# Optimization experiments

Measured on AMD Instinct MI355X. Metric: run time of the kernel, lower is better.

## Reference

```python
import jax, jax.numpy as jnp
import numpy as np

B, N, C, H = 2, 2048, 1024, 16
D = C // H          # head dim = 64
HID = 4 * C         # MLP hidden = 4096
LN_EPS = 1e-5
ROPE_BASE = 10000.0


def layernorm(x, g, b):
    mu = jnp.mean(x, axis=-1, keepdims=True)
    var = jnp.var(x, axis=-1, keepdims=True)
    return (x - mu) * jax.lax.rsqrt(var + LN_EPS) * g + b


def rotate_half(x):
    # interleaved pairs: (x0, x1) -> (-x1, x0), lucidrains rotary_embedding_torch style
    x = x.reshape(*x.shape[:-1], -1, 2)
    x1, x2 = x[..., 0], x[..., 1]
    return jnp.stack([-x2, x1], axis=-1).reshape(*x.shape[:-2], -1)


def rope_cos_sin(n, d, dtype):
    inv_freq = 1.0 / (ROPE_BASE ** (jnp.arange(0, d, 2, dtype=jnp.float32) / d))
    ang = jnp.arange(n, dtype=jnp.float32)[:, None] * inv_freq          # [N, D/2]
    ang = jnp.repeat(ang, 2, axis=-1)                                    # [N, D] interleaved
    return jnp.cos(ang).astype(dtype), jnp.sin(ang).astype(dtype)


def setup_inputs() -> dict:
    key = jax.random.key(0)
    ks = jax.random.split(key, 16)
    s = 0.02
    return {
        "x": jax.random.normal(ks[0], (B, N, C), jnp.float32),
        "ln1_g": jnp.ones((C,), jnp.float32),
        "ln1_b": jnp.zeros((C,), jnp.float32),
        "qkv_w": jax.random.normal(ks[1], (C, 3 * C), jnp.float32) * s,   # stored [in, out]
        "qkv_b": jnp.zeros((3 * C,), jnp.float32),
        "proj_w": jax.random.normal(ks[2], (C, C), jnp.float32) * s,
        "proj_b": jnp.zeros((C,), jnp.float32),
        "ln2_g": jnp.ones((C,), jnp.float32),
        "ln2_b": jnp.zeros((C,), jnp.float32),
        "fc1_w": jax.random.normal(ks[3], (C, HID), jnp.float32) * s,
        "fc1_b": jnp.zeros((HID,), jnp.float32),
        "ffn_ln_g": jnp.ones((HID,), jnp.float32),
        "ffn_ln_b": jnp.zeros((HID,), jnp.float32),
        "fc2_w": jax.random.normal(ks[4], (HID, C), jnp.float32) * s,
        "fc2_b": jnp.zeros((C,), jnp.float32),
    }


def reference(x, ln1_g, ln1_b, qkv_w, qkv_b, proj_w, proj_b,
              ln2_g, ln2_b, fc1_w, fc1_b, ffn_ln_g, ffn_ln_b, fc2_w, fc2_b):
    b, n, c = x.shape
    h, d = H, c // H
    scale = d ** -0.5

    # --- attention branch (pre-norm) ---
    hx = layernorm(x, ln1_g, ln1_b)
    qkv = hx @ qkv_w + qkv_b                                   # [B,N,3C]
    qkv = qkv.reshape(b, n, 3, h, d).transpose(2, 0, 3, 1, 4)  # [3,B,H,N,D]
    q, k, v = qkv[0], qkv[1], qkv[2]

    cos, sin = rope_cos_sin(n, d, x.dtype)                     # [N,D]
    q = q * cos + rotate_half(q) * sin
    k = k * cos + rotate_half(k) * sin

    attn = jax.nn.softmax(jnp.einsum('bhqd,bhkd->bhqk', q, k) * scale, axis=-1)
    o = jnp.einsum('bhqk,bhkd->bhqd', attn, v)                 # [B,H,N,D]
    o = o.transpose(0, 2, 1, 3).reshape(b, n, c)               # B N (H D)
    x = x + o @ proj_w + proj_b

    # --- MLP branch (pre-norm; GELU then LayerNorm on hidden, per FeedForwardBlock) ---
    m = layernorm(x, ln2_g, ln2_b)
    m = jax.nn.gelu(m @ fc1_w + fc1_b, approximate=False)
    m = layernorm(m, ffn_ln_g, ffn_ln_b)
    m = m @ fc2_w + fc2_b
    return x + m
```

## Files before the change

### kernel.cpp

```cpp
#include <hip/hip_runtime.h>
#include <hip/hip_bf16.h>
#include <cmath>

typedef __bf16 bf16_t;
typedef __bf16 bf16x8 __attribute__((ext_vector_type(8)));
typedef float f32x4 __attribute__((ext_vector_type(4)));
typedef float f32x16 __attribute__((ext_vector_type(16)));
typedef unsigned short u16;
typedef unsigned int u32;
typedef unsigned int u32x2 __attribute__((ext_vector_type(2)));

#if defined(__has_builtin)
#if __has_builtin(__builtin_amdgcn_exp2f)
#define ATTN_EXP(x) __builtin_amdgcn_exp2f(x)
#define ATTN_LOG2E 1.4426950408889634f
#define HAVE_EXP2 1
#endif
#if __has_builtin(__builtin_amdgcn_permlane32_swap)
#define HAVE_PL32 1
#endif
#if __has_builtin(__builtin_amdgcn_rcpf)
#define FAST_RCP(x) __builtin_amdgcn_rcpf(x)
#endif
#endif
#ifndef ATTN_EXP
#define ATTN_EXP(x) __expf(x)
#define ATTN_LOG2E 1.0f
#endif
#ifndef FAST_RCP
#define FAST_RCP(x) (1.0f / (x))
#endif

__device__ __forceinline__ float fast_gelu(float v) {
#ifdef HAVE_EXP2
  float u = v * __builtin_fmaf(0.044715f, v * v, 1.0f);
  float z = __builtin_amdgcn_exp2f(-2.3022163968f * u);
  return v * FAST_RCP(1.0f + z);
#else
  return 0.5f * v * (1.0f + erff(v * 0.70710678118654752f));
#endif
}

__device__ __forceinline__ void load16(const bf16_t* g, bf16_t* l) {
  __builtin_amdgcn_global_load_lds((const __attribute__((address_space(1))) u32*)g,
                                   (__attribute__((address_space(3))) u32*)l, 16, 0, 0);
}

__device__ __forceinline__ u32 pk2(float a, float b) {
  bf16_t x = (bf16_t)a, y = (bf16_t)b;
  u16 ux = __builtin_bit_cast(u16, x), uy = __builtin_bit_cast(u16, y);
  return (u32)ux | ((u32)uy << 16);
}

union V4U { u32 w[4]; bf16x8 v; };

__device__ __forceinline__ void pl32(u32 a, u32 b, u32& out_lo, u32& out_hi) {
#ifdef HAVE_PL32
  u32x2 r = __builtin_amdgcn_permlane32_swap(a, b, false, false);
  out_lo = r[0];
  out_hi = r[1];
#else
  u32 ax = (u32)__shfl_xor((int)a, 32), bx = (u32)__shfl_xor((int)b, 32);
  out_lo = (threadIdx.x & 32) ? bx : a;
  out_hi = (threadIdx.x & 32) ? b : ax;
#endif
}

__device__ __forceinline__ float pl32_sum(float x) {
  u32 lo, hi;
  pl32(__builtin_bit_cast(u32, x), __builtin_bit_cast(u32, x), lo, hi);
  return __builtin_bit_cast(float, lo) + __builtin_bit_cast(float, hi);
}

__device__ __forceinline__ void tr64(const float* __restrict__ src, bf16_t* __restrict__ dst,
                                     int Kd, int Nd, int ntile, int ktile, int tid) {
  __shared__ float tile[64][68];
  int n0 = ntile * 64, k0 = ktile * 64;
  int r = tid >> 2, c4 = (tid & 3) * 4;
  const float* sp = src + (size_t)(k0 + r) * Nd + n0;
#pragma unroll
  for (int c = 0; c < 4; ++c)
    *(float4*)&tile[r][c * 16 + c4] = *(const float4*)(sp + c * 16 + c4);
  __syncthreads();
  int n = tid >> 2;
  bf16_t* dp = dst + (size_t)(n0 + n) * Kd + k0;
#pragma unroll
  for (int c = 0; c < 4; ++c) {
    int kk = c * 16 + c4;
    uint2 pk;
    pk.x = pk2(tile[kk + 0][n], tile[kk + 1][n]);
    pk.y = pk2(tile[kk + 2][n], tile[kk + 3][n]);
    *(uint2*)(dp + kk) = pk;
  }
}

__global__ __launch_bounds__(256) void prep_kernel(
    const float* __restrict__ qkv_w, const float* __restrict__ proj_w,
    const float* __restrict__ fc1_w, const float* __restrict__ fc2_w,
    bf16_t* __restrict__ qkvT, bf16_t* __restrict__ projT,
    bf16_t* __restrict__ fc1T, bf16_t* __restrict__ fc2T,
    float* __restrict__ ropeC, float* __restrict__ ropeS) {
  int b = blockIdx.x, tid = threadIdx.x;
  if (b < 768) {
    tr64(qkv_w, qkvT, 1024, 3072, b % 48, b / 48, tid);
  } else if (b < 1024) {
    int r = b - 768; tr64(proj_w, projT, 1024, 1024, r % 16, r / 16, tid);
  } else if (b < 2048) {
    int r = b - 1024; tr64(fc1_w, fc1T, 1024, 4096, r % 64, r / 64, tid);
  } else if (b < 3072) {
    int r = b - 2048; tr64(fc2_w, fc2T, 4096, 1024, r % 16, r / 16, tid);
  } else {
    int idx = (b - 3072) * 256 + tid;
    int pos = idx >> 5, t = idx & 31;
    float e = (float)(2 * t) / 64.0f;
    float inv = powf(10000.0f, -e);
    float a = (float)pos * inv;
    ropeC[idx] = cosf(a);
    ropeS[idx] = sinf(a);
  }
}

template <typename TI, int W>
__global__ __launch_bounds__(256) void ln_kernel(const TI* __restrict__ in,
                                                 const float* __restrict__ g,
                                                 const float* __restrict__ b,
                                                 bf16_t* __restrict__ out) {
  constexpr int CH = (sizeof(TI) == 2) ? 8 : 4;
  constexpr int NS = W / (256 * CH);
  int row = blockIdx.x;
  const TI* p = in + (size_t)row * W;
  float vals[NS * CH];
  float s = 0.f, q = 0.f;
#pragma unroll
  for (int sw = 0; sw < NS; ++sw) {
    int base = sw * (256 * CH) + threadIdx.x * CH;
    if constexpr (sizeof(TI) == 2) {
      bf16x8 v = *(const bf16x8*)(p + base);
#pragma unroll
      for (int e = 0; e < 8; ++e) {
        float f = (float)v[e];
        vals[sw * CH + e] = f; s += f; q += f * f;
      }
    } else {
      float4 v = *(const float4*)(p + base);
      float f0 = v.x, f1 = v.y, f2 = v.z, f3 = v.w;
      vals[sw * CH + 0] = f0; vals[sw * CH + 1] = f1;
      vals[sw * CH + 2] = f2; vals[sw * CH + 3] = f3;
      s += (f0 + f1) + (f2 + f3);
      q += (f0 * f0 + f1 * f1) + (f2 * f2 + f3 * f3);
    }
  }
  for (int off = 32; off; off >>= 1) { s += __shfl_xor(s, off); q += __shfl_xor(q, off); }
  __shared__ float red[8];
  int wave = threadIdx.x >> 6, lane = threadIdx.x & 63;
  if (lane == 0) { red[wave] = s; red[4 + wave] = q; }
  __syncthreads();
  s = red[0] + red[1] + red[2] + red[3];
  q = red[4] + red[5] + red[6] + red[7];
  float mu = s * (1.0f / W);
  float var = q * (1.0f / W) - mu * mu;
  float rstd = rsqrtf(var + 1e-5f);
  bf16_t* op = out + (size_t)row * W;
#pragma unroll
  for (int sw = 0; sw < NS; ++sw) {
    int base = sw * (256 * CH) + threadIdx.x * CH;
    float o[CH];
#pragma unroll
    for (int e = 0; e < CH; ++e)
      o[e] = (vals[sw * CH + e] - mu) * rstd * g[base + e] + b[base + e];
    if constexpr (CH == 8) {
      V4U u;
      u.w[0] = pk2(o[0], o[1]); u.w[1] = pk2(o[2], o[3]);
      u.w[2] = pk2(o[4], o[5]); u.w[3] = pk2(o[6], o[7]);
      *(bf16x8*)(op + base) = u.v;
    } else {
      uint2 pk; pk.x = pk2(o[0], o[1]); pk.y = pk2(o[2], o[3]);
      *(uint2*)(op + base) = pk;
    }
  }
}

template <int NS>
__global__ __launch_bounds__(256) void reduceN_kernel(
    const float* __restrict__ part, const float* __restrict__ resid,
    const float* __restrict__ bias, float* __restrict__ out) {
  const int total4 = (4096 * 1024) / 4;
  const float4* r4 = (const float4*)resid;
  const float4* b4 = (const float4*)bias;
  float4* o4 = (float4*)out;
  for (int i = blockIdx.x * 256 + threadIdx.x; i < total4; i += gridDim.x * 256) {
    float4 a = ((const float4*)part)[i];
#pragma unroll
    for (int s = 1; s < NS; ++s) {
      float4 p = ((const float4*)(part + (size_t)s * 4096 * 1024))[i];
      a.x += p.x; a.y += p.y; a.z += p.z; a.w += p.w;
    }
    float4 r = r4[i], bb = b4[i & 255];
    float4 o;
    o.x = a.x + (r.x + bb.x);
    o.y = a.y + (r.y + bb.y);
    o.z = a.z + (r.z + bb.z);
    o.w = a.w + (r.w + bb.w);
    o4[i] = o;
  }
}

enum { EPI_QKV = 0, EPI_RESID = 1, EPI_GELU = 2, EPI_PART = 3 };

template <int EPI, int TM>
__global__ __launch_bounds__(256, 2) void gemm_bt(
    const bf16_t* __restrict__ A, const bf16_t* __restrict__ Bt, int M, int Nn, int K,
    int gy, int ksteps,
    const float* __restrict__ bias, const float* __restrict__ resid,
    float* __restrict__ outf, bf16_t* __restrict__ outb,
    bf16_t* __restrict__ qb, bf16_t* __restrict__ kb, bf16_t* __restrict__ vtb,
    const float* __restrict__ ropeC, const float* __restrict__ ropeS) {
  constexpr int MT = TM / 32;
  __shared__ bf16_t lsA[2][TM * 32];
  __shared__ bf16_t lsB[2][128 * 32];
  const int tid = threadIdx.x;
  const int lane = tid & 63;
  const int wave = tid >> 6;
  const int l16 = lane & 15, quad = lane >> 4;
  const int wm = (wave >> 1) * (TM / 2), wn = (wave & 1) * 64;
  const int bb = blockIdx.x;
  const int m0 = (bb % gy) * TM, n0 = (bb / gy) * 128;
  const int kbase = blockIdx.y * (ksteps << 5);

  f32x4 acc[MT][4];
  for (int i = 0; i < MT; ++i)
    for (int j = 0; j < 4; ++j) acc[i][j] = {0.f, 0.f, 0.f, 0.f};

  auto stage = [&](int kk, int buf) {
    bf16_t* la = &lsA[buf][0];
    bf16_t* lb = &lsB[buf][0];
#pragma unroll
    for (int i = 0; i < TM / 64; ++i) {
      int s = tid + i * 256;
      int row = s >> 2, ch = (s & 3) ^ (row & 3);
      load16(A + (size_t)(m0 + row) * K + kk + ch * 8, la + s * 8);
    }
#pragma unroll
    for (int i = 0; i < 2; ++i) {
      int s = tid + i * 256;
      int row = s >> 2, ch = (s & 3) ^ (row & 3);
      load16(Bt + (size_t)(n0 + row) * K + kk + ch * 8, lb + s * 8);
    }
  };

  stage(kbase, 0);
  for (int ki = 0; ki < ksteps; ++ki) {
    __syncthreads();
    if (ki + 1 < ksteps) stage(kbase + ((ki + 1) << 5), (ki + 1) & 1);
    const bf16_t* la = &lsA[ki & 1][0];
    const bf16_t* lb = &lsB[ki & 1][0];
    bf16x8 af[MT], bfr[4];
#pragma unroll
    for (int t = 0; t < MT; ++t) {
      int row = wm + t * 16 + l16;
      af[t] = *(const bf16x8*)(la + row * 32 + (quad ^ (row & 3)) * 8);
    }
#pragma unroll
    for (int t = 0; t < 4; ++t) {
      int row = wn + t * 16 + l16;
      bfr[t] = *(const bf16x8*)(lb + row * 32 + (quad ^ (row & 3)) * 8);
    }
#pragma unroll
    for (int mt = 0; mt < MT; ++mt)
#pragma unroll
      for (int nt = 0; nt < 4; ++nt)
        acc[mt][nt] = __builtin_amdgcn_mfma_f32_16x16x32_bf16(af[mt], bfr[nt], acc[mt][nt], 0, 0, 0);
  }

  for (int mt = 0; mt < MT; ++mt) {
    for (int nt = 0; nt < 4; ++nt) {
      int gn = n0 + wn + nt * 16 + l16;
      int gm0 = m0 + wm + mt * 16 + quad * 4;
      if constexpr (EPI == EPI_QKV) {
        int which = gn >> 10;
        int hd = gn & 1023, head = hd >> 6, d = hd & 63;
        if (which == 2) {
          u32 lo, hi;
          {
            float v0 = acc[mt][nt][0] + bias[gn];
            float v1 = acc[mt][nt][1] + bias[gn];
            float v2 = acc[mt][nt][2] + bias[gn];
            float v3 = acc[mt][nt][3] + bias[gn];
            lo = pk2(v0, v1);
            hi = pk2(v2, v3);
          }
          int b = gm0 >> 11, pos = gm0 & 2047;
          int bh = b * 16 + head;
          uint2 pk; pk.x = lo; pk.y = hi;
          *(uint2*)(vtb + ((size_t)bh * 64 + d) * 2048 + pos) = pk;
        } else {
          bf16_t* dst = (which == 0) ? qb : kb;
          int t = d >> 1;
          for (int r = 0; r < 4; ++r) {
            float v = acc[mt][nt][r] + bias[gn];
            float pn = __shfl_xor(v, 1);
            int gm = gm0 + r;
            int b = gm >> 11, pos = gm & 2047;
            float cc = ropeC[pos * 32 + t], ss = ropeS[pos * 32 + t];
            float o = (d & 1) ? (v * cc + pn * ss) : (v * cc - pn * ss);
            dst[(((size_t)(b * 16 + head)) * 2048 + pos) * 64 + d] = (bf16_t)o;
          }
        }
      } else if constexpr (EPI == EPI_GELU) {
        for (int r = 0; r < 4; ++r) {
          int gm = gm0 + r;
          float v = acc[mt][nt][r] + bias[gn];
          outb[(size_t)gm * Nn + gn] = (bf16_t)fast_gelu(v);
        }
      } else if constexpr (EPI == EPI_PART) {
        float* po = outf + (size_t)blockIdx.y * M * Nn;
        for (int r = 0; r < 4; ++r) {
          int gm = gm0 + r;
          po[(size_t)gm * Nn + gn] = acc[mt][nt][r];
        }
      } else {
        for (int r = 0; r < 4; ++r) {
          int gm = gm0 + r;
          size_t idx = (size_t)gm * Nn + gn;
          outf[idx] = acc[mt][nt][r] + bias[gn] + resid[idx];
        }
      }
    }
  }
}

__global__ __launch_bounds__(256, 2) void attn_kernel(
    const bf16_t* __restrict__ q, const bf16_t* __restrict__ k,
    const bf16_t* __restrict__ vt, bf16_t* __restrict__ o) {
  __shared__ bf16_t lsK[2][128 * 64];
  __shared__ bf16_t lsV[2][64 * 128];

  const int tid = threadIdx.x, lane = tid & 63, wave = tid >> 6;
  const int c31 = lane & 31, hi = lane >> 5, h7 = c31 & 7;
  const int bh = blockIdx.y, qt = blockIdx.x;
  const int b = bh >> 4, h = bh & 15;
  const bf16_t* qp = q + (size_t)bh * 2048 * 64;
  const bf16_t* kp = k + (size_t)bh * 2048 * 64;
  const bf16_t* vp = vt + (size_t)bh * 64 * 2048;
  const int qrow0 = qt * 128 + wave * 32;
  const int qrow = qrow0 + c31;

  const float QS = 0.125f * ATTN_LOG2E;
  bf16x8 qb[4];
#pragma unroll
  for (int ks = 0; ks < 4; ++ks) {
    bf16x8 t = *(const bf16x8*)(qp + (size_t)qrow * 64 + ks * 16 + hi * 8);
#pragma unroll
    for (int j = 0; j < 8; ++j) t[j] = (bf16_t)((float)t[j] * QS);
    qb[ks] = t;
  }

  f32x16 oacc[2];
  oacc[0] = 0.f; oacc[1] = 0.f;
  float lstate = 0.f;

  auto stage = [&](int kt, int buf) {
    const bf16_t* kg = kp + (size_t)kt * 128 * 64;
    bf16_t* lk = &lsK[buf][0];
    bf16_t* lv = &lsV[buf][0];
#pragma unroll
    for (int i = 0; i < 4; ++i) {
      int s = tid + i * 256;
      int kr = s >> 3, kc = (s & 7) ^ (kr & 7);
      load16(kg + (size_t)kr * 64 + kc * 8, lk + s * 8);
      int vr = s >> 4, vc = (s & 15) ^ (vr & 7);
      load16(vp + (size_t)vr * 2048 + kt * 128 + vc * 8, lv + s * 8);
    }
  };

  stage(0, 0);
  for (int kt = 0; kt < 16; ++kt) {
    __syncthreads();
    if (kt < 15) stage(kt + 1, (kt + 1) & 1);
    const bf16_t* lk = &lsK[kt & 1][0];
    const bf16_t* lv = &lsV[kt & 1][0];

    f32x16 sacc[4];
    sacc[0] = 0.f; sacc[1] = 0.f; sacc[2] = 0.f; sacc[3] = 0.f;
    __builtin_amdgcn_s_setprio(1);
#pragma unroll
    for (int ks = 0; ks < 4; ++ks) {
      int cs = ((ks * 2 + hi) ^ h7) * 8;
#pragma unroll
      for (int nt = 0; nt < 4; ++nt) {
        bf16x8 kf = *(const bf16x8*)(lk + (nt * 32 + c31) * 64 + cs);
        sacc[nt] = __builtin_amdgcn_mfma_f32_32x32x16_bf16(kf, qb[ks], sacc[nt], 0, 0, 0);
      }
    }
    __builtin_amdgcn_s_setprio(0);

    float rsn[4];
    u32 u[4][4][2];
#pragma unroll
    for (int nt = 0; nt < 4; ++nt) {
      float a0 = 0.f, a1 = 0.f;
#pragma unroll
      for (int t = 0; t < 4; ++t) {
        float p0 = ATTN_EXP(sacc[nt][4 * t + 0]);
        float p1 = ATTN_EXP(sacc[nt][4 * t + 1]);
        float p2 = ATTN_EXP(sacc[nt][4 * t + 2]);
        float p3 = ATTN_EXP(sacc[nt][4 * t + 3]);
        a0 += p0 + p1; a1 += p2 + p3;
        u[nt][t][0] = pk2(p0, p1);
        u[nt][t][1] = pk2(p2, p3);
      }
      rsn[nt] = a0 + a1;
    }
    float rs = (rsn[0] + rsn[1]) + (rsn[2] + rsn[3]);
    rs = pl32_sum(rs);
    lstate += rs;

    __builtin_amdgcn_s_setprio(1);
#pragma unroll
    for (int ks = 0; ks < 8; ++ks) {
      int n = ks >> 1, t0 = (ks & 1) * 2;
      V4U f;
      pl32(u[n][t0][0], u[n][t0 + 1][0], f.w[0], f.w[2]);
      pl32(u[n][t0][1], u[n][t0 + 1][1], f.w[1], f.w[3]);
      bf16x8 pf = f.v;
      int cs = ((ks * 2 + hi) ^ h7) * 8;
#pragma unroll
      for (int dt = 0; dt < 2; ++dt) {
        bf16x8 vf = *(const bf16x8*)(lv + (dt * 32 + c31) * 128 + cs);
        oacc[dt] = __builtin_amdgcn_mfma_f32_32x32x16_bf16(vf, pf, oacc[dt], 0, 0, 0);
      }
    }
    __builtin_amdgcn_s_setprio(0);
  }

  float inv = 1.0f / lstate;
  bf16_t* orow = o + ((size_t)(b * 2048 + qrow)) * 1024 + h * 64;
#pragma unroll
  for (int dt = 0; dt < 2; ++dt)
#pragma unroll
    for (int t = 0; t < 4; ++t) {
      int d0 = dt * 32 + 8 * t + 4 * hi;
      uint2 pk;
      pk.x = pk2(oacc[dt][4 * t + 0] * inv, oacc[dt][4 * t + 1] * inv);
      pk.y = pk2(oacc[dt][4 * t + 2] * inv, oacc[dt][4 * t + 3] * inv);
      *(uint2*)(orow + d0) = pk;
    }
}

extern "C" void kernel_launch(void* const* d_in, const int* in_sizes, int n_in,
                              void* d_out, int out_size, void* d_ws, size_t ws_size,
                              hipStream_t stream) {
  const float* x = (const float*)d_in[0];
  const float* ln1_g = (const float*)d_in[1];
  const float* ln1_b = (const float*)d_in[2];
  const float* qkv_w = (const float*)d_in[3];
  const float* qkv_b = (const float*)d_in[4];
  const float* proj_w = (const float*)d_in[5];
  const float* proj_b = (const float*)d_in[6];
  const float* ln2_g = (const float*)d_in[7];
  const float* ln2_b = (const float*)d_in[8];
  const float* fc1_w = (const float*)d_in[9];
  const float* fc1_b = (const float*)d_in[10];
  const float* ffg = (const float*)d_in[11];
  const float* ffb = (const float*)d_in[12];
  const float* fc2_w = (const float*)d_in[13];
  const float* fc2_b = (const float*)d_in[14];
  float* out = (float*)d_out;

  char* ws = (char*)d_ws;
  size_t off = 0;
  auto alloc = [&](size_t n) { char* p = ws + off; off += (n + 255) & ~(size_t)255; return p; };

  bf16_t* qkvT  = (bf16_t*)alloc(3072ull * 1024 * 2);
  bf16_t* projT = (bf16_t*)alloc(1024ull * 1024 * 2);
  bf16_t* fc1T  = (bf16_t*)alloc(4096ull * 1024 * 2);
  bf16_t* fc2T  = (bf16_t*)alloc(1024ull * 4096 * 2);
  float*  ropeC = (float*)alloc(2048ull * 32 * 4);
  float*  ropeS = (float*)alloc(2048ull * 32 * 4);
  bf16_t* hx    = (bf16_t*)alloc(4096ull * 1024 * 2);
  bf16_t* qbuf  = (bf16_t*)alloc(32ull * 2048 * 64 * 2);
  bf16_t* kbuf  = (bf16_t*)alloc(32ull * 2048 * 64 * 2);
  bf16_t* vtbuf = (bf16_t*)alloc(32ull * 64 * 2048 * 2);
  bf16_t* obuf  = (bf16_t*)alloc(4096ull * 1024 * 2);
  float*  x2    = (float*)alloc(4096ull * 1024 * 4);
  bf16_t* h1    = (bf16_t*)alloc(4096ull * 4096 * 2);
  bf16_t* hln   = (bf16_t*)qbuf;

  const size_t part4_bytes = 4ull * 4096 * 1024 * 4;
  float* part;
  int nsplit;
  if (off + part4_bytes <= ws_size) {
    part = (float*)alloc(part4_bytes);
    nsplit = 4;
  } else {
    part = (float*)h1;
    nsplit = 2;
  }

  prep_kernel<<<3328, 256, 0, stream>>>(qkv_w, proj_w, fc1_w, fc2_w,
                                        qkvT, projT, fc1T, fc2T, ropeC, ropeS);

  ln_kernel<float, 1024><<<4096, 256, 0, stream>>>(x, ln1_g, ln1_b, hx);
  gemm_bt<EPI_QKV, 128><<<768, 256, 0, stream>>>(hx, qkvT, 4096, 3072, 1024, 32, 32, qkv_b,
      nullptr, nullptr, nullptr, qbuf, kbuf, vtbuf, ropeC, ropeS);
  attn_kernel<<<dim3(16, 32), 256, 0, stream>>>(qbuf, kbuf, vtbuf, obuf);
  gemm_bt<EPI_RESID, 64><<<512, 256, 0, stream>>>(obuf, projT, 4096, 1024, 1024, 64, 32,
      proj_b, x, x2, nullptr, nullptr, nullptr, nullptr, nullptr, nullptr);
  ln_kernel<float, 1024><<<4096, 256, 0, stream>>>(x2, ln2_g, ln2_b, hx);
  gemm_bt<EPI_GELU, 128><<<1024, 256, 0, stream>>>(hx, fc1T, 4096, 4096, 1024, 32, 32, fc1_b,
      nullptr, nullptr, h1, nullptr, nullptr, nullptr, nullptr, nullptr);
  ln_kernel<bf16_t, 4096><<<4096, 256, 0, stream>>>(h1, ffg, ffb, hln);
  gemm_bt<EPI_PART, 128><<<dim3(256, nsplit), 256, 0, stream>>>(hln, fc2T, 4096, 1024, 4096,
      32, 128 / nsplit, nullptr, nullptr, part, nullptr, nullptr, nullptr, nullptr,
      nullptr, nullptr);
  if (nsplit == 4)
    reduceN_kernel<4><<<2048, 256, 0, stream>>>(part, x2, fc2_b, out);
  else
    reduceN_kernel<2><<<2048, 256, 0, stream>>>(part, x2, fc2_b, out);
}
```

Before: 372.7 us.

## Single-buffer V in LDS via register staging to raise attention occupancy

```diff
diff --git a/kernel.cpp b/kernel.cpp
--- a/kernel.cpp
+++ b/kernel.cpp
@@ -329,11 +329,11 @@
   }
 }
 
-__global__ __launch_bounds__(256, 2) void attn_kernel(
+__global__ __launch_bounds__(256, 3) void attn_kernel(
     const bf16_t* __restrict__ q, const bf16_t* __restrict__ k,
     const bf16_t* __restrict__ vt, bf16_t* __restrict__ o) {
   __shared__ bf16_t lsK[2][128 * 64];
-  __shared__ bf16_t lsV[2][64 * 128];
+  __shared__ bf16_t lsV[64 * 128];
 
   const int tid = threadIdx.x, lane = tid & 63, wave = tid >> 6;
   const int c31 = lane & 31, hi = lane >> 5, h7 = c31 & 7;
@@ -359,26 +359,45 @@
   oacc[0] = 0.f; oacc[1] = 0.f;
   float lstate = 0.f;
 
-  auto stage = [&](int kt, int buf) {
+  auto stage_k = [&](int kt, int buf) {
     const bf16_t* kg = kp + (size_t)kt * 128 * 64;
     bf16_t* lk = &lsK[buf][0];
-    bf16_t* lv = &lsV[buf][0];
 #pragma unroll
     for (int i = 0; i < 4; ++i) {
       int s = tid + i * 256;
       int kr = s >> 3, kc = (s & 7) ^ (kr & 7);
       load16(kg + (size_t)kr * 64 + kc * 8, lk + s * 8);
+    }
+  };
+  auto load_v = [&](int kt, bf16x8* vr4) {
+#pragma unroll
+    for (int i = 0; i < 4; ++i) {
+      int s = tid + i * 256;
       int vr = s >> 4, vc = (s & 15) ^ (vr & 7);
-      load16(vp + (size_t)vr * 2048 + kt * 128 + vc * 8, lv + s * 8);
+      vr4[i] = *(const bf16x8*)(vp + (size_t)vr * 2048 + kt * 128 + vc * 8);
     }
   };
-
-  stage(0, 0);
+  auto write_v = [&](const bf16x8* vr4) {
+#pragma unroll
+    for (int i = 0; i < 4; ++i) {
+      int s = tid + i * 256;
+      *(bf16x8*)(&lsV[s * 8]) = vr4[i];
+    }
+  };
+
+  bf16x8 vreg[4];
+  stage_k(0, 0);
+  load_v(0, vreg);
+  __syncthreads();
+  write_v(vreg);
+  __syncthreads();
+
   for (int kt = 0; kt < 16; ++kt) {
-    __syncthreads();
-    if (kt < 15) stage(kt + 1, (kt + 1) & 1);
+    if (kt < 15) {
+      stage_k(kt + 1, (kt + 1) & 1);
+      load_v(kt + 1, vreg);
+    }
     const bf16_t* lk = &lsK[kt & 1][0];
-    const bf16_t* lv = &lsV[kt & 1][0];
 
     f32x16 sacc[4];
     sacc[0] = 0.f; sacc[1] = 0.f; sacc[2] = 0.f; sacc[3] = 0.f;
@@ -426,11 +445,17 @@
       int cs = ((ks * 2 + hi) ^ h7) * 8;
 #pragma unroll
       for (int dt = 0; dt < 2; ++dt) {
-        bf16x8 vf = *(const bf16x8*)(lv + (dt * 32 + c31) * 128 + cs);
+        bf16x8 vf = *(const bf16x8*)(&lsV[(dt * 32 + c31) * 128 + cs]);
         oacc[dt] = __builtin_amdgcn_mfma_f32_32x32x16_bf16(vf, pf, oacc[dt], 0, 0, 0);
       }
     }
     __builtin_amdgcn_s_setprio(0);
+
+    if (kt < 15) {
+      __syncthreads();
+      write_v(vreg);
+      __syncthreads();
+    }
   }
 
   float inv = 1.0f / lstate;
@@ -485,17 +510,7 @@
   float*  x2    = (float*)alloc(4096ull * 1024 * 4);
   bf16_t* h1    = (bf16_t*)alloc(4096ull * 4096 * 2);
   bf16_t* hln   = (bf16_t*)qbuf;
-
-  const size_t part4_bytes = 4ull * 4096 * 1024 * 4;
-  float* part;
-  int nsplit;
-  if (off + part4_bytes <= ws_size) {
-    part = (float*)alloc(part4_bytes);
-    nsplit = 4;
-  } else {
-    part = (float*)h1;
-    nsplit = 2;
-  }
+  float*  part  = (float*)h1;
 
   prep_kernel<<<3328, 256, 0, stream>>>(qkv_w, proj_w, fc1_w, fc2_w,
                                         qkvT, projT, fc1T, fc2T, ropeC, ropeS);
@@ -510,11 +525,7 @@
   gemm_bt<EPI_GELU, 128><<<1024, 256, 0, stream>>>(hx, fc1T, 4096, 4096, 1024, 32, 32, fc1_b,
       nullptr, nullptr, h1, nullptr, nullptr, nullptr, nullptr, nullptr);
   ln_kernel<bf16_t, 4096><<<4096, 256, 0, stream>>>(h1, ffg, ffb, hln);
-  gemm_bt<EPI_PART, 128><<<dim3(256, nsplit), 256, 0, stream>>>(hln, fc2T, 4096, 1024, 4096,
-      32, 128 / nsplit, nullptr, nullptr, part, nullptr, nullptr, nullptr, nullptr,
-      nullptr, nullptr);
-  if (nsplit == 4)
-    reduceN_kernel<4><<<2048, 256, 0, stream>>>(part, x2, fc2_b, out);
-  else
-    reduceN_kernel<2><<<2048, 256, 0, stream>>>(part, x2, fc2_b, out);
-}
+  gemm_bt<EPI_PART, 128><<<dim3(256, 2), 256, 0, stream>>>(hln, fc2T, 4096, 1024, 4096,
+      32, 64, nullptr, nullptr, part, nullptr, nullptr, nullptr, nullptr, nullptr, nullptr);
+  reduceN_kernel<2><<<2048, 256, 0, stream>>>(part, x2, fc2_b, out);
+}
```

After: 444.8 us. 1.19x slower.
